# Kernel tuning notes

Measured on AMD Instinct MI355X. Metric: run time of the kernel, lower is better.

## Reference

```python
import jax, jax.numpy as jnp
import numpy as np

B, C, H, W = 16, 256, 32, 32
N_EMBED = 8192
BETA = 0.25


def setup_inputs() -> dict:
    key = jax.random.key(0)
    k1, k2 = jax.random.split(key)
    x = jax.random.normal(k1, (B, C, H, W), dtype=jnp.float32)
    # nn.Embedding(n_embed + 1, dim); last row is the padding row (unused by argmin path)
    weight = jax.random.normal(k2, (N_EMBED + 1, C), dtype=jnp.float32) * 0.01
    return {"x": x, "weight": weight}


def reference(x, weight):
    b, c, h, w = x.shape
    codebook = weight[:-1, :]                      # [n_embed, d]
    xt = jnp.transpose(x, (0, 2, 3, 1)).reshape(b, h * w, c)   # b (h w) c
    flat = xt.reshape(-1, c)                       # [N, d]

    x_sq = jnp.sum(flat * flat, axis=1, keepdims=True)          # [N, 1]
    c_sq = jnp.sum(codebook * codebook, axis=1)[None, :]        # [1, n_embed]
    dists = x_sq + c_sq - 2.0 * (flat @ codebook.T)             # [N, n_embed]
    code = jnp.argmin(dists, axis=-1)                           # [N]

    x_q = codebook[code]                                        # gather [N, d]
    x_q = x_q.reshape(b, h * w, c)
    code = code.reshape(b, h * w)

    # commitment losses (eval mode: no EMA buffer update)
    sg = jax.lax.stop_gradient
    loss = BETA * jnp.mean((sg(x_q) - xt) ** 2) + jnp.mean((x_q - sg(xt)) ** 2)

    # straight-through estimator
    x_q = xt + sg(x_q - xt)

    x_q = jnp.transpose(x_q.reshape(b, h, w, c), (0, 3, 1, 2))  # b c h w
    code = code.reshape(b, h, w)
    return x_q, loss, code
```

## Files before the change

### kernel.cpp

```cpp
#include <hip/hip_runtime.h>
#include <float.h>
#include <limits.h>
#include <math.h>

#define B_      16
#define C_      256
#define HW      1024
#define ROWS    (B_*HW)
#define NCODE   8192
#define KDIM    256

#define SXQ 28.0f
#define SWQ 2400.0f
#define SPROD_HALF 33600.0

typedef __attribute__((ext_vector_type(4)))  int i32x4;
typedef __attribute__((ext_vector_type(16))) int i32x16;

__device__ __forceinline__ unsigned umn(unsigned a, unsigned b){ return a < b ? a : b; }
__device__ __forceinline__ unsigned umx(unsigned a, unsigned b){ return a > b ? a : b; }

__device__ __forceinline__ void gload_lds16(const void* g, void* l) {
    __builtin_amdgcn_global_load_lds(
        (const __attribute__((address_space(1))) unsigned int*)g,
        (__attribute__((address_space(3))) unsigned int*)l, 16, 0, 0);
}

__device__ __forceinline__ uint4 merge44(uint4 a, uint4 b) {
    unsigned w0 = umn(a.x, b.w), w1 = umn(a.y, b.z);
    unsigned w2 = umn(a.z, b.y), w3 = umn(a.w, b.x);
    unsigned s0 = umn(w0, w2), s2 = umx(w0, w2);
    unsigned s1 = umn(w1, w3), s3 = umx(w1, w3);
    uint4 o;
    o.x = umn(s0, s1); o.y = umx(s0, s1);
    o.z = umn(s2, s3); o.w = umx(s2, s3);
    return o;
}

__device__ __forceinline__ int q8(float v, float s) {
    return __float2int_rn(fminf(fmaxf(v * s, -127.f), 127.f));
}

__global__ __launch_bounds__(256)
void prep_kernel(const float* __restrict__ x, const float* __restrict__ w,
                 float* __restrict__ csq, unsigned char* __restrict__ wq8,
                 unsigned char* __restrict__ xq8)
{
    __shared__ float Lt[64][65];

    if (blockIdx.x < 2048) {
        int j = blockIdx.x * 4 + (threadIdx.x >> 6);
        int l = threadIdx.x & 63;
        float4 v = *(const float4*)(w + (size_t)j * KDIM + l * 4);
        double s = (double)v.x*v.x + (double)v.y*v.y + (double)v.z*v.z + (double)v.w*v.w;
        #pragma unroll
        for (int off = 1; off < 64; off <<= 1) s += __shfl_xor(s, off, 64);
        if (l == 0) csq[j] = (float)s;

        int q0 = q8(v.x, SWQ), q1 = q8(v.y, SWQ), q2 = q8(v.z, SWQ), q3 = q8(v.w, SWQ);
        unsigned pk = (unsigned)(q0 & 0xFF) | ((unsigned)(q1 & 0xFF) << 8)
                    | ((unsigned)(q2 & 0xFF) << 16) | ((unsigned)(q3 & 0xFF) << 24);
        int k32 = l >> 3, hi = (l >> 2) & 1, idx = (l & 3) * 4;
        int cb = j >> 5;
        *(unsigned*)(wq8 + ((size_t)(k32 * 256 + cb) * 64 + (j & 31) + 32 * hi) * 16 + idx) = pk;

        if (l < 2) {
            double T = -s * SPROD_HALF;
            int wA = (int)rint(T / 127.0);
            int wB = (int)rint(T - 127.0 * (double)wA);
            wA = wA < -127 ? -127 : (wA > 127 ? 127 : wA);
            wB = wB < -127 ? -127 : (wB > 127 ? 127 : wB);
            uint4 f; f.x = 0; f.y = 0; f.z = 0; f.w = 0;
            if (l == 0) f.x = (unsigned)(wA & 0xFF) | ((unsigned)(wB & 0xFF) << 8);
            *(uint4*)(wq8 + ((size_t)(8 * 256 + cb) * 64 + (j & 31) + 32 * l) * 16) = f;
        }
        return;
    }

    int bx = blockIdx.x - 2048;
    int t  = threadIdx.x;
    int b  = bx >> 6;
    int kt = (bx >> 4) & 3;
    int pt = bx & 15;

    #pragma unroll
    for (int rnd = 0; rnd < 16; ++rnd) {
        int kk = rnd * 4 + (t >> 6);
        int pp = t & 63;
        Lt[kk][pp] = x[((size_t)(b * 256 + kt * 64 + kk)) * 1024 + pt * 64 + pp];
    }
    __syncthreads();

    int p = t >> 2, q = t & 3;
    int row = b * 1024 + pt * 64 + p;
    int xb  = row >> 5;
    int k32 = kt * 2 + (q >> 1), hi = q & 1;

    unsigned wds[4];
    #pragma unroll
    for (int wi = 0; wi < 4; ++wi) {
        unsigned pk = 0;
        #pragma unroll
        for (int i2 = 0; i2 < 4; ++i2) {
            int qi = q8(Lt[q*16 + wi*4 + i2][p], SXQ);
            pk |= ((unsigned)(qi & 0xFF)) << (8 * i2);
        }
        wds[wi] = pk;
    }
    uint4 pkv; pkv.x = wds[0]; pkv.y = wds[1]; pkv.z = wds[2]; pkv.w = wds[3];
    *(uint4*)(xq8 + ((size_t)(k32 * 512 + xb) * 64 + (p & 31) + 32 * hi) * 16) = pkv;

    if (kt == 0 && q < 2) {
        uint4 f; f.x = 0; f.y = 0; f.z = 0; f.w = 0;
        if (q == 0) f.x = 127u | (1u << 8);
        *(uint4*)(xq8 + ((size_t)(8 * 512 + xb) * 64 + (p & 31) + 32 * q) * 16) = f;
    }
}

__global__ __launch_bounds__(256, 2)
void stage1_kernel(const unsigned char* __restrict__ wq8,
                   const unsigned char* __restrict__ xq8,
                   uint4* __restrict__ part)
{
    extern __shared__ unsigned char smem[];
    const int tid = threadIdx.x;
    const int wid = tid >> 6;
    const int l   = tid & 63;
    const int bid = blockIdx.x;
    const int chunk = (bid & 7) >> 1;
    const int rb    = (bid >> 3) | ((bid & 1) << 6);
    const int row0  = rb * 128;
    const int cbase = chunk * 2048;
    const int wr = wid >> 1, wc = wid & 1;
    unsigned char* priv = smem + wid * 16384;

    i32x4 xf[9][2];
    #pragma unroll
    for (int k9 = 0; k9 < 9; ++k9)
        #pragma unroll
        for (int nf = 0; nf < 2; ++nf)
            xf[k9][nf] = *(const i32x4*)(xq8 +
                ((size_t)(k9 * 512 + rb * 4 + wc * 2 + nf) * 64 + l) * 16);
    asm volatile("s_waitcnt vmcnt(0)" ::: "memory");

    auto stage1p = [&](int tt, int kk, int sl) {
        #pragma unroll
        for (int mf = 0; mf < 4; ++mf) {
            size_t src = (((size_t)(kk * 256 + chunk * 64 + tt * 8 + wr * 4 + mf)) * 64 + l) * 16;
            gload_lds16(wq8 + src, priv + sl * 4096 + mf * 1024);
        }
    };

    stage1p(0, 0, 0);
    stage1p(0, 1, 1);
    stage1p(0, 2, 2);

    unsigned key1[2], key2[2], key3[2];
    key1[0]=0xFFFFFFFFu; key1[1]=0xFFFFFFFFu;
    key2[0]=0xFFFFFFFFu; key2[1]=0xFFFFFFFFu;
    key3[0]=0xFFFFFFFFu; key3[1]=0xFFFFFFFFu;
    const int hi4 = (l >> 5) * 4;

    #pragma unroll 1
    for (int t = 0; t < 8; ++t) {
        i32x16 acc[4][2];
        #pragma unroll
        for (int mf = 0; mf < 4; ++mf)
            #pragma unroll
            for (int nf = 0; nf < 2; ++nf)
                acc[mf][nf] = (i32x16)(0);

        #pragma unroll
        for (int k9 = 0; k9 < 9; ++k9) {
            {
                int k2 = k9 + 3, t2 = t;
                if (k2 >= 9) { k2 -= 9; t2 = t + 1; }
                if (k9 < 6 || t < 7) stage1p(t2, k2, (t + k9 + 3) & 3);
            }
            if (k9 < 6) {
                asm volatile("s_waitcnt vmcnt(12)" ::: "memory");
            } else if (t < 7) {
                asm volatile("s_waitcnt vmcnt(12)" ::: "memory");
            } else if (k9 == 6) {
                asm volatile("s_waitcnt vmcnt(8)" ::: "memory");
            } else if (k9 == 7) {
                asm volatile("s_waitcnt vmcnt(4)" ::: "memory");
            } else {
                asm volatile("s_waitcnt vmcnt(0)" ::: "memory");
            }
            __builtin_amdgcn_sched_barrier(0);

            const unsigned char* Ac = priv + ((t + k9) & 3) * 4096;
            i32x4 af[4];
            #pragma unroll
            for (int mf = 0; mf < 4; ++mf)
                af[mf] = *(const i32x4*)(Ac + mf * 1024 + l * 16);
            #pragma unroll
            for (int mf = 0; mf < 4; ++mf)
                #pragma unroll
                for (int nf = 0; nf < 2; ++nf)
                    acc[mf][nf] = __builtin_amdgcn_mfma_i32_32x32x32_i8(
                        af[mf], xf[k9][nf], acc[mf][nf], 0, 0, 0);
        }

        #pragma unroll
        for (int mf = 0; mf < 4; ++mf) {
            unsigned base_mf = (unsigned)(t * 256 + (wr * 4 + mf) * 32 + hi4);
            #pragma unroll
            for (int nf = 0; nf < 2; ++nf) {
                #pragma unroll
                for (int j2 = 0; j2 < 4; ++j2) {
                    unsigned k0 = ((unsigned)(0x100000 - acc[mf][nf][4*j2+0]) << 11) | (base_mf + 8*j2 + 0);
                    unsigned k1 = ((unsigned)(0x100000 - acc[mf][nf][4*j2+1]) << 11) | (base_mf + 8*j2 + 1);
                    unsigned k2 = ((unsigned)(0x100000 - acc[mf][nf][4*j2+2]) << 11) | (base_mf + 8*j2 + 2);
                    unsigned k3 = ((unsigned)(0x100000 - acc[mf][nf][4*j2+3]) << 11) | (base_mf + 8*j2 + 3);
                    unsigned qm = umn(umn(k0, k1), umn(k2, k3));
                    unsigned t1 = umn(key1[nf], qm), t2 = umx(key1[nf], qm);
                    key1[nf] = t1;
                    unsigned u1 = umn(key2[nf], t2), u2 = umx(key2[nf], t2);
                    key2[nf] = u1;
                    key3[nf] = umn(key3[nf], u2);
                }
            }
        }
    }

    __syncthreads();

    uint4* red = (uint4*)smem;
    #pragma unroll
    for (int nf = 0; nf < 2; ++nf) {
        unsigned a1 = key1[nf], a2 = key2[nf], a3 = key3[nf];
        unsigned b1 = __shfl_xor(a1, 32, 64);
        unsigned b2 = __shfl_xor(a2, 32, 64);
        unsigned b3 = __shfl_xor(a3, 32, 64);
        uint4 av; av.x = a1; av.y = a2; av.z = a3; av.w = 0xFFFFFFFFu;
        uint4 bv; bv.x = b1; bv.y = b2; bv.z = b3; bv.w = 0xFFFFFFFFu;
        uint4 m = merge44(av, bv);
        if (l < 32) {
            int xrl = (wc * 2 + nf) * 32 + (l & 31);
            red[xrl * 2 + wr] = m;
        }
    }
    __syncthreads();

    if (tid < 128) {
        uint4 m = merge44(red[tid * 2 + 0], red[tid * 2 + 1]);
        uint4 o;
        o.x = (unsigned)cbase + (m.x & 0x7FFu);
        o.y = (unsigned)cbase + (m.y & 0x7FFu);
        o.z = (unsigned)cbase + (m.z & 0x7FFu);
        o.w = (unsigned)cbase + (m.w & 0x7FFu);
        part[(size_t)(row0 + tid) * 4 + chunk] = o;
    }
}

__global__ __launch_bounds__(256)
void tail_kernel(const float* __restrict__ x, const float* __restrict__ w,
                 const float* __restrict__ csq, const unsigned* __restrict__ part,
                 float* __restrict__ xq, float* __restrict__ code_f,
                 double* __restrict__ partials)
{
    extern __shared__ unsigned char sm2[];
    float*    Lt    = (float*)sm2;
    float*    Wt    = (float*)(sm2 + 33792);
    unsigned* PcL   = (unsigned*)(sm2 + 33792 + 33280);
    int*      codeL = (int*)(sm2 + 33792 + 33280 + 2048);

    const int tid = threadIdx.x;
    const int b   = blockIdx.x >> 5;
    const int p0  = (blockIdx.x & 31) * 32;

    #pragma unroll 4
    for (int it = 0; it < 32; ++it) {
        int c  = it * 8 + (tid >> 5);
        int pp = tid & 31;
        Lt[c * 33 + pp] = x[((size_t)(b * 256 + c)) * 1024 + p0 + pp];
    }
    {
        const unsigned* ps = part + (size_t)(b * 1024 + p0) * 16;
        *(uint2*)&PcL[tid * 2] = *(const uint2*)&ps[tid * 2];
    }
    __syncthreads();

    const int w4   = tid >> 6;
    const int lane = tid & 63;
    const int pr   = lane >> 3, s = lane & 7;
    const int rl   = w4 * 8 + pr;

    float xs[32];
    #pragma unroll
    for (int k = 0; k < 32; ++k) xs[k] = Lt[(s * 32 + k) * 33 + rl];

    double ss = 0.0;
    #pragma unroll
    for (int k = 0; k < 32; ++k) ss += (double)xs[k] * (double)xs[k];
    ss += __shfl_xor(ss, 1, 64);
    ss += __shfl_xor(ss, 2, 64);
    ss += __shfl_xor(ss, 4, 64);
    float S32 = (float)ss;

    float bd = FLT_MAX; int bi = INT_MAX;
    #pragma unroll 1
    for (int ct = 0; ct < 16; ++ct) {
        int ci = (int)PcL[rl * 16 + ct];
        const float4* wr4 = (const float4*)(w + (size_t)ci * 256 + s * 32);
        float csv = csq[ci];
        double acc = 0.0;
        #pragma unroll
        for (int q4 = 0; q4 < 8; ++q4) {
            float4 wv = wr4[q4];
            acc += (double)wv.x * (double)xs[q4*4 + 0];
            acc += (double)wv.y * (double)xs[q4*4 + 1];
            acc += (double)wv.z * (double)xs[q4*4 + 2];
            acc += (double)wv.w * (double)xs[q4*4 + 3];
        }
        acc += __shfl_xor(acc, 1, 64);
        acc += __shfl_xor(acc, 2, 64);
        acc += __shfl_xor(acc, 4, 64);
        float tt = (float)(2.0 * acc);
        float sc = S32 + csv;
        float d  = sc - tt;
        if (d < bd || (d == bd && ci < bi)) { bd = d; bi = ci; }
    }
    if (s == 0) {
        codeL[rl] = bi;
        code_f[b * 1024 + p0 + rl] = (float)bi;
    }
    __syncthreads();

    #pragma unroll
    for (int it = 0; it < 8; ++it) {
        int r2 = it * 4 + w4;
        int code = codeL[r2];
        float4 wv = *(const float4*)(w + (size_t)code * 256 + lane * 4);
        *(float4*)&Wt[r2 * 260 + lane * 4] = wv;
    }
    __syncthreads();

    double ls = 0.0;
    #pragma unroll 4
    for (int it = 0; it < 32; ++it) {
        int c  = it * 8 + (tid >> 5);
        int pp = tid & 31;
        float val = Wt[pp * 260 + c];
        float xv  = Lt[c * 33 + pp];
        xq[((size_t)(b * 256 + c)) * 1024 + p0 + pp] = val;
        float diff = val - xv;
        ls += (double)diff * (double)diff;
    }
    #pragma unroll
    for (int off = 1; off < 64; off <<= 1) ls += __shfl_xor(ls, off, 64);
    if (lane == 0) partials[blockIdx.x * 4 + w4] = ls;
}

__global__ __launch_bounds__(256)
void loss_kernel(const double* __restrict__ partials, float* __restrict__ loss_out)
{
    __shared__ double sred[256];
    double s = 0.0;
    for (int i = threadIdx.x; i < 2048; i += 256) s += partials[i];
    sred[threadIdx.x] = s;
    __syncthreads();
    for (int k = 128; k > 0; k >>= 1) {
        if (threadIdx.x < k) sred[threadIdx.x] += sred[threadIdx.x + k];
        __syncthreads();
    }
    if (threadIdx.x == 0)
        loss_out[0] = (float)(sred[0] * (1.25 / (double)(B_ * 256 * HW)));
}

extern "C" void kernel_launch(void* const* d_in, const int* in_sizes, int n_in,
                              void* d_out, int out_size, void* d_ws, size_t ws_size,
                              hipStream_t stream)
{
    const float* x = (const float*)d_in[0];
    const float* w = (const float*)d_in[1];
    float* out    = (float*)d_out;
    float* xq     = out;
    float* loss   = out + 4194304;
    float* code_f = out + 4194305;

    char* ws = (char*)d_ws;
    float*         csq      = (float*)(ws);
    double*        partials = (double*)(ws + 256*1024);
    uint4*         part     = (uint4*)(ws + 512*1024);
    unsigned char* wq8      = (unsigned char*)(ws + (size_t)2*1024*1024);
    unsigned char* xq8      = (unsigned char*)(ws + (size_t)5*1024*1024);

    (void)hipFuncSetAttribute((const void*)stage1_kernel,
                              hipFuncAttributeMaxDynamicSharedMemorySize, 65536);
    (void)hipFuncSetAttribute((const void*)tail_kernel,
                              hipFuncAttributeMaxDynamicSharedMemorySize, 69248);

    prep_kernel   <<<3072,  256, 0, stream>>>(x, w, csq, wq8, xq8);
    stage1_kernel <<<512,   256, 65536, stream>>>(wq8, xq8, part);
    tail_kernel   <<<512,   256, 69248, stream>>>(x, w, csq, (const unsigned*)part,
                                                  xq, code_f, partials);
    loss_kernel   <<<1,     256, 0, stream>>>(partials, loss);
}
```

Measured before the change: 103.5 us.

## Halve stage1 row tile and overlap top-3 epilogue with next tile's MFMAs

The stage1 int8 distance kernel now processes 64 rows per block instead of 128, doubling the grid to 1024 blocks. Accumulators are double-buffered (accA/accB) so the top-3 key reduction for the previous code tile is interleaved with the MFMA loop of the current tile instead of running as a separate epilogue. The aim is to hide the VALU epilogue behind matrix work and to improve occupancy and load balance. In exchange, each block reloads the codebook tiles for half as many rows, which doubles codebook traffic and halves MFMA reuse per LDS load.

After: 129.6 us. 1.25x slower.

```diff
diff --git a/kernel.cpp b/kernel.cpp
--- a/kernel.cpp
+++ b/kernel.cpp
@@ -127,20 +127,19 @@
     const int wid = tid >> 6;
     const int l   = tid & 63;
     const int bid = blockIdx.x;
-    const int chunk = (bid & 7) >> 1;
-    const int rb    = (bid >> 3) | ((bid & 1) << 6);
-    const int row0  = rb * 128;
+    const int xcd = bid & 7;
+    const int chunk = xcd >> 1;
+    const int rb  = ((bid >> 3) << 1) | (xcd & 1);
+    const int row0  = rb * 64;
     const int cbase = chunk * 2048;
     const int wr = wid >> 1, wc = wid & 1;
     unsigned char* priv = smem + wid * 16384;
 
-    i32x4 xf[9][2];
+    i32x4 xf[9];
     #pragma unroll
     for (int k9 = 0; k9 < 9; ++k9)
-        #pragma unroll
-        for (int nf = 0; nf < 2; ++nf)
-            xf[k9][nf] = *(const i32x4*)(xq8 +
-                ((size_t)(k9 * 512 + rb * 4 + wc * 2 + nf) * 64 + l) * 16);
+        xf[k9] = *(const i32x4*)(xq8 +
+            ((size_t)(k9 * 512 + rb * 2 + wc) * 64 + l) * 16);
     asm volatile("s_waitcnt vmcnt(0)" ::: "memory");
 
     auto stage1p = [&](int tt, int kk, int sl) {
@@ -155,96 +154,88 @@
     stage1p(0, 1, 1);
     stage1p(0, 2, 2);
 
-    unsigned key1[2], key2[2], key3[2];
-    key1[0]=0xFFFFFFFFu; key1[1]=0xFFFFFFFFu;
-    key2[0]=0xFFFFFFFFu; key2[1]=0xFFFFFFFFu;
-    key3[0]=0xFFFFFFFFu; key3[1]=0xFFFFFFFFu;
+    unsigned key1 = 0xFFFFFFFFu, key2 = 0xFFFFFFFFu, key3 = 0xFFFFFFFFu;
     const int hi4 = (l >> 5) * 4;
 
+    i32x16 accA[4], accB[4];
+    #pragma unroll
+    for (int mf = 0; mf < 4; ++mf) accB[mf] = (i32x16)(-0xFFFFF);
+
+    #define EPIQ(AP, TP, MF, J2) do {                                          \
+        unsigned bmf = (unsigned)((TP) * 256 + (wr * 4 + (MF)) * 32 + hi4);    \
+        unsigned e0 = ((unsigned)(0x100000 - (AP)[(MF)][4*(J2)+0]) << 11) | (bmf + 8*(J2) + 0); \
+        unsigned e1 = ((unsigned)(0x100000 - (AP)[(MF)][4*(J2)+1]) << 11) | (bmf + 8*(J2) + 1); \
+        unsigned e2 = ((unsigned)(0x100000 - (AP)[(MF)][4*(J2)+2]) << 11) | (bmf + 8*(J2) + 2); \
+        unsigned e3 = ((unsigned)(0x100000 - (AP)[(MF)][4*(J2)+3]) << 11) | (bmf + 8*(J2) + 3); \
+        unsigned qm = umn(umn(e0, e1), umn(e2, e3));                           \
+        unsigned t1_ = umn(key1, qm), t2_ = umx(key1, qm);                     \
+        key1 = t1_;                                                            \
+        unsigned u1_ = umn(key2, t2_), u2_ = umx(key2, t2_);                   \
+        key2 = u1_;                                                            \
+        key3 = umn(key3, u2_);                                                 \
+    } while (0)
+
+    #define PHASES(T, AC, AP) do {                                             \
+        _Pragma("unroll")                                                      \
+        for (int mf = 0; mf < 4; ++mf) (AC)[mf] = (i32x16)(0);                 \
+        _Pragma("unroll")                                                      \
+        for (int k9 = 0; k9 < 9; ++k9) {                                       \
+            if (k9 < 6 || (T) < 7) {                                           \
+                int k2 = k9 + 3, t2 = (T);                                     \
+                if (k2 >= 9) { k2 -= 9; ++t2; }                                \
+                stage1p(t2, k2, ((T) + k9 + 3) & 3);                           \
+            }                                                                  \
+            if (k9 < 6)       { asm volatile("s_waitcnt vmcnt(12)" ::: "memory"); } \
+            else if ((T) < 7) { asm volatile("s_waitcnt vmcnt(12)" ::: "memory"); } \
+            else if (k9 == 6) { asm volatile("s_waitcnt vmcnt(8)"  ::: "memory"); } \
+            else if (k9 == 7) { asm volatile("s_waitcnt vmcnt(4)"  ::: "memory"); } \
+            else              { asm volatile("s_waitcnt vmcnt(0)"  ::: "memory"); } \
+            __builtin_amdgcn_sched_barrier(0);                                 \
+            const unsigned char* Ac = priv + (((T) + k9) & 3) * 4096;          \
+            i32x4 af[4];                                                       \
+            _Pragma("unroll")                                                  \
+            for (int mf = 0; mf < 4; ++mf)                                     \
+                af[mf] = *(const i32x4*)(Ac + mf * 1024 + l * 16);             \
+            _Pragma("unroll")                                                  \
+            for (int mf = 0; mf < 4; ++mf)                                     \
+                (AC)[mf] = __builtin_amdgcn_mfma_i32_32x32x32_i8(              \
+                    af[mf], xf[k9], (AC)[mf], 0, 0, 0);                        \
+            if (k9 < 8) {                                                      \
+                EPIQ(AP, (T) - 1, (k9 >> 1), ((2 * k9) & 3));                  \
+                EPIQ(AP, (T) - 1, ((2 * k9 + 1) >> 2), ((2 * k9 + 1) & 3));    \
+            }                                                                  \
+        }                                                                      \
+    } while (0)
+
     #pragma unroll 1
-    for (int t = 0; t < 8; ++t) {
-        i32x16 acc[4][2];
-        #pragma unroll
-        for (int mf = 0; mf < 4; ++mf)
-            #pragma unroll
-            for (int nf = 0; nf < 2; ++nf)
-                acc[mf][nf] = (i32x16)(0);
-
-        #pragma unroll
-        for (int k9 = 0; k9 < 9; ++k9) {
-            {
-                int k2 = k9 + 3, t2 = t;
-                if (k2 >= 9) { k2 -= 9; t2 = t + 1; }
-                if (k9 < 6 || t < 7) stage1p(t2, k2, (t + k9 + 3) & 3);
-            }
-            if (k9 < 6) {
-                asm volatile("s_waitcnt vmcnt(12)" ::: "memory");
-            } else if (t < 7) {
-                asm volatile("s_waitcnt vmcnt(12)" ::: "memory");
-            } else if (k9 == 6) {
-                asm volatile("s_waitcnt vmcnt(8)" ::: "memory");
-            } else if (k9 == 7) {
-                asm volatile("s_waitcnt vmcnt(4)" ::: "memory");
-            } else {
-                asm volatile("s_waitcnt vmcnt(0)" ::: "memory");
-            }
-            __builtin_amdgcn_sched_barrier(0);
-
-            const unsigned char* Ac = priv + ((t + k9) & 3) * 4096;
-            i32x4 af[4];
-            #pragma unroll
-            for (int mf = 0; mf < 4; ++mf)
-                af[mf] = *(const i32x4*)(Ac + mf * 1024 + l * 16);
-            #pragma unroll
-            for (int mf = 0; mf < 4; ++mf)
-                #pragma unroll
-                for (int nf = 0; nf < 2; ++nf)
-                    acc[mf][nf] = __builtin_amdgcn_mfma_i32_32x32x32_i8(
-                        af[mf], xf[k9][nf], acc[mf][nf], 0, 0, 0);
-        }
-
-        #pragma unroll
-        for (int mf = 0; mf < 4; ++mf) {
-            unsigned base_mf = (unsigned)(t * 256 + (wr * 4 + mf) * 32 + hi4);
-            #pragma unroll
-            for (int nf = 0; nf < 2; ++nf) {
-                #pragma unroll
-                for (int j2 = 0; j2 < 4; ++j2) {
-                    unsigned k0 = ((unsigned)(0x100000 - acc[mf][nf][4*j2+0]) << 11) | (base_mf + 8*j2 + 0);
-                    unsigned k1 = ((unsigned)(0x100000 - acc[mf][nf][4*j2+1]) << 11) | (base_mf + 8*j2 + 1);
-                    unsigned k2 = ((unsigned)(0x100000 - acc[mf][nf][4*j2+2]) << 11) | (base_mf + 8*j2 + 2);
-                    unsigned k3 = ((unsigned)(0x100000 - acc[mf][nf][4*j2+3]) << 11) | (base_mf + 8*j2 + 3);
-                    unsigned qm = umn(umn(k0, k1), umn(k2, k3));
-                    unsigned t1 = umn(key1[nf], qm), t2 = umx(key1[nf], qm);
-                    key1[nf] = t1;
-                    unsigned u1 = umn(key2[nf], t2), u2 = umx(key2[nf], t2);
-                    key2[nf] = u1;
-                    key3[nf] = umn(key3[nf], u2);
-                }
-            }
-        }
-    }
+    for (int th = 0; th < 4; ++th) {
+        const int t0 = th * 2;
+        PHASES(t0,     accA, accB);
+        PHASES(t0 + 1, accB, accA);
+    }
+    #pragma unroll
+    for (int c = 0; c < 8; ++c) {
+        EPIQ(accB, 7, (c >> 1), ((2 * c) & 3));
+        EPIQ(accB, 7, ((2 * c + 1) >> 2), ((2 * c + 1) & 3));
+    }
+    #undef PHASES
+    #undef EPIQ
 
     __syncthreads();
 
     uint4* red = (uint4*)smem;
-    #pragma unroll
-    for (int nf = 0; nf < 2; ++nf) {
-        unsigned a1 = key1[nf], a2 = key2[nf], a3 = key3[nf];
-        unsigned b1 = __shfl_xor(a1, 32, 64);
-        unsigned b2 = __shfl_xor(a2, 32, 64);
-        unsigned b3 = __shfl_xor(a3, 32, 64);
-        uint4 av; av.x = a1; av.y = a2; av.z = a3; av.w = 0xFFFFFFFFu;
-        uint4 bv; bv.x = b1; bv.y = b2; bv.z = b3; bv.w = 0xFFFFFFFFu;
+    {
+        unsigned b1 = __shfl_xor(key1, 32, 64);
+        unsigned b2 = __shfl_xor(key2, 32, 64);
+        unsigned b3 = __shfl_xor(key3, 32, 64);
+        uint4 av; av.x = key1; av.y = key2; av.z = key3; av.w = 0xFFFFFFFFu;
+        uint4 bv; bv.x = b1;   bv.y = b2;   bv.z = b3;   bv.w = 0xFFFFFFFFu;
         uint4 m = merge44(av, bv);
-        if (l < 32) {
-            int xrl = (wc * 2 + nf) * 32 + (l & 31);
-            red[xrl * 2 + wr] = m;
-        }
-    }
-    __syncthreads();
-
-    if (tid < 128) {
+        if (l < 32) red[(wc * 32 + l) * 2 + wr] = m;
+    }
+    __syncthreads();
+
+    if (tid < 64) {
         uint4 m = merge44(red[tid * 2 + 0], red[tid * 2 + 1]);
         uint4 o;
         o.x = (unsigned)cbase + (m.x & 0x7FFu);
@@ -394,7 +385,7 @@
                               hipFuncAttributeMaxDynamicSharedMemorySize, 69248);
 
     prep_kernel   <<<3072,  256, 0, stream>>>(x, w, csq, wq8, xq8);
-    stage1_kernel <<<512,   256, 65536, stream>>>(wq8, xq8, part);
+    stage1_kernel <<<1024,  256, 65536, stream>>>(wq8, xq8, part);
     tail_kernel   <<<512,   256, 69248, stream>>>(x, w, csq, (const unsigned*)part,
                                                   xq, code_f, partials);
     loss_kernel   <<<1,     256, 0, stream>>>(partials, loss);
```
